# Optimization experiments

Hardware: AMD Instinct MI355X
Metric: run time of the kernel (lower is better)

## Reference

```python
import jax, jax.numpy as jnp
import numpy as np

D_MODEL = 1024
NUM_HEADS = 16
D_K = D_MODEL // NUM_HEADS


def setup_inputs() -> dict:
    key = jax.random.key(0)
    ks = jax.random.split(key, 9)
    B, S = 2, 2048
    s_in = 1.0 / np.sqrt(D_MODEL)
    x = jax.random.normal(ks[0], (B, S, D_MODEL), dtype=jnp.float32)
    # Linear weights stored as (in_features, out_features): y = x @ W + b
    Wq = jax.random.uniform(ks[1], (D_MODEL, D_MODEL), jnp.float32, -s_in, s_in)
    bq = jax.random.uniform(ks[2], (D_MODEL,), jnp.float32, -s_in, s_in)
    Wk = jax.random.uniform(ks[3], (D_MODEL, D_K), jnp.float32, -s_in, s_in)
    bk = jax.random.uniform(ks[4], (D_K,), jnp.float32, -s_in, s_in)
    Wv = jax.random.uniform(ks[5], (D_MODEL, D_K), jnp.float32, -s_in, s_in)
    bv = jax.random.uniform(ks[6], (D_K,), jnp.float32, -s_in, s_in)
    Wo = jax.random.uniform(ks[7], (D_MODEL, D_MODEL), jnp.float32, -s_in, s_in)
    bo = jax.random.uniform(ks[8], (D_MODEL,), jnp.float32, -s_in, s_in)
    return {"x": x, "Wq": Wq, "bq": bq, "Wk": Wk, "bk": bk,
            "Wv": Wv, "bv": bv, "Wo": Wo, "bo": bo}


def reference(x, Wq, bq, Wk, bk, Wv, bv, Wo, bo):
    B, S, _ = x.shape
    H, Dk = NUM_HEADS, D_K
    # Projections
    Q = (x @ Wq + bq).reshape(B, S, H, Dk).transpose(0, 2, 1, 3)  # [B,H,S,Dk]
    K = x @ Wk + bk                                               # [B,S,Dk] single KV head
    V = x @ Wv + bv                                               # [B,S,Dk]
    # Scores: query heads broadcast against the single shared KV head
    scores = jnp.einsum('bhqd,bkd->bhqk', Q, K) / jnp.sqrt(jnp.float32(Dk))
    attn = jax.nn.softmax(scores, axis=-1)                        # [B,H,S,S]
    out = jnp.einsum('bhqk,bkd->bhqd', attn, V)                   # [B,H,S,Dk]
    out = out.transpose(0, 2, 1, 3).reshape(B, S, H * Dk)         # [B,S,d_model]
    return out @ Wo + bo
```

## Files before the change

kernel.cpp:

```cpp
#include <hip/hip_runtime.h>

typedef __attribute__((ext_vector_type(8))) short bf16x8;
typedef __attribute__((ext_vector_type(4))) float f32x4;
typedef __attribute__((ext_vector_type(16))) float f32x16;
typedef __attribute__((ext_vector_type(4))) unsigned short ushort4v;

#define QSCALE 0.1803368801111204f

__device__ __forceinline__ unsigned short f2bf(float f) {
  union { float f; unsigned int u; } x; x.f = f;
  unsigned int u = x.u;
  unsigned int r = (u + 0x7fffu + ((u >> 16) & 1u)) >> 16;
  return (unsigned short)r;
}

__global__ __launch_bounds__(256) void cvt_bf16_kernel(
    const float* __restrict__ in, unsigned short* __restrict__ out, int n) {
  int i = (blockIdx.x * 256 + threadIdx.x) * 4;
  if (i + 3 < n) {
    float4 v = *(const float4*)(in + i);
    ushort4v o = { f2bf(v.x), f2bf(v.y), f2bf(v.z), f2bf(v.w) };
    *(ushort4v*)(out + i) = o;
  }
}

__global__ __launch_bounds__(256) void transpose_cvt_fused(
    const float* __restrict__ Wq, const float* __restrict__ Wk,
    const float* __restrict__ Wv, const float* __restrict__ Wo,
    unsigned short* __restrict__ QKVt, unsigned short* __restrict__ Wot) {
  __shared__ float t[32][33];
  int z = blockIdx.z;
  const float* src;
  unsigned short* dst;
  int C, rowoff;
  if (z == 0)      { src = Wq; dst = QKVt; C = 1024; rowoff = 0; }
  else if (z == 1) { src = Wk; dst = QKVt; C = 64;   rowoff = 1024; }
  else if (z == 2) { src = Wv; dst = QKVt; C = 64;   rowoff = 1088; }
  else             { src = Wo; dst = Wot;  C = 1024; rowoff = 0; }
  int c0 = blockIdx.x * 32, r0 = blockIdx.y * 32;
  if (c0 >= C) return;
  int tx = threadIdx.x & 31, ty = threadIdx.x >> 5;
#pragma unroll
  for (int i = 0; i < 32; i += 8)
    t[ty + i][tx] = src[(size_t)(r0 + ty + i) * C + c0 + tx];
  __syncthreads();
#pragma unroll
  for (int i = 0; i < 32; i += 8)
    dst[(size_t)(rowoff + c0 + ty + i) * 1024 + r0 + tx] = f2bf(t[tx][ty + i]);
}

__global__ __launch_bounds__(256) void make_vt_kernel(
    const unsigned short* __restrict__ QKV, unsigned short* __restrict__ Vt) {
  __shared__ unsigned short t[32][33];
  int b = blockIdx.z;
  int s0 = blockIdx.x * 32, d0 = blockIdx.y * 32;
  int tx = threadIdx.x & 31, ty = threadIdx.x >> 5;
#pragma unroll
  for (int i = 0; i < 32; i += 8)
    t[ty + i][tx] = QKV[(size_t)(b * 2048 + s0 + ty + i) * 1152 + 1088 + d0 + tx];
  __syncthreads();
#pragma unroll
  for (int i = 0; i < 32; i += 8)
    Vt[((size_t)b * 64 + d0 + ty + i) * 2048 + s0 + tx] = t[tx][ty + i];
}

template <typename OutT, bool QKVMODE>
__global__ __launch_bounds__(256) void gemm_bf16_kernel(
    const unsigned short* __restrict__ A, const unsigned short* __restrict__ Bt,
    const float* __restrict__ b0, const float* __restrict__ b1,
    const float* __restrict__ b2, OutT* __restrict__ C, int M, int N, int K) {
  constexpr int LS = 40;
  __shared__ unsigned short As[2][128 * LS];
  __shared__ unsigned short Bs[2][128 * LS];
  int tid = threadIdx.x;
  int wid = tid >> 6, lane = tid & 63;
  int l15 = lane & 15, quad = lane >> 4;
  int m0 = blockIdx.x * 128, n0 = blockIdx.y * 128;
  int mw = (wid >> 1) * 64, nw = (wid & 1) * 64;
  f32x4 acc[4][4];
#pragma unroll
  for (int i = 0; i < 4; i++)
#pragma unroll
    for (int j = 0; j < 4; j++)
#pragma unroll
      for (int e = 0; e < 4; ++e) acc[i][j][e] = 0.f;

  int arow = tid >> 2, akc = (tid & 3) * 8;
  const unsigned short* Ag = A + (size_t)(m0 + arow) * K + akc;
  const unsigned short* Bg = Bt + (size_t)(n0 + arow) * K + akc;
  bf16x8 ar0 = *(const bf16x8*)(Ag);
  bf16x8 ar1 = *(const bf16x8*)(Ag + (size_t)64 * K);
  bf16x8 br0 = *(const bf16x8*)(Bg);
  bf16x8 br1 = *(const bf16x8*)(Bg + (size_t)64 * K);

  for (int k0 = 0; k0 < K; k0 += 32) {
    unsigned short* Asb = As[(k0 >> 5) & 1];
    unsigned short* Bsb = Bs[(k0 >> 5) & 1];
    *(bf16x8*)(Asb + arow * LS + akc) = ar0;
    *(bf16x8*)(Asb + (arow + 64) * LS + akc) = ar1;
    *(bf16x8*)(Bsb + arow * LS + akc) = br0;
    *(bf16x8*)(Bsb + (arow + 64) * LS + akc) = br1;
    __syncthreads();
    if (k0 + 32 < K) {
      ar0 = *(const bf16x8*)(Ag + k0 + 32);
      ar1 = *(const bf16x8*)(Ag + (size_t)64 * K + k0 + 32);
      br0 = *(const bf16x8*)(Bg + k0 + 32);
      br1 = *(const bf16x8*)(Bg + (size_t)64 * K + k0 + 32);
    }
    bf16x8 af[4], bfr[4];
#pragma unroll
    for (int t = 0; t < 4; ++t)
      af[t] = *(const bf16x8*)(Asb + (mw + t * 16 + l15) * LS + quad * 8);
#pragma unroll
    for (int t = 0; t < 4; ++t)
      bfr[t] = *(const bf16x8*)(Bsb + (nw + t * 16 + l15) * LS + quad * 8);
#pragma unroll
    for (int mt = 0; mt < 4; ++mt)
#pragma unroll
      for (int nt = 0; nt < 4; ++nt)
        acc[mt][nt] = __builtin_amdgcn_mfma_f32_16x16x32_bf16(
            af[mt], bfr[nt], acc[mt][nt], 0, 0, 0);
  }
#pragma unroll
  for (int mt = 0; mt < 4; ++mt)
#pragma unroll
    for (int nt = 0; nt < 4; ++nt) {
      int col = n0 + nw + nt * 16 + l15;
      float bias, cs;
      if constexpr (QKVMODE) {
        bias = (col < 1024) ? b0[col] : ((col < 1088) ? b1[col - 1024] : b2[col - 1088]);
        cs = (col < 1024) ? QSCALE : 1.0f;
      } else {
        bias = b0[col];
        cs = 1.0f;
      }
#pragma unroll
      for (int r = 0; r < 4; ++r) {
        int row = m0 + mw + mt * 16 + quad * 4 + r;
        float v = (acc[mt][nt][r] + bias) * cs;
        if constexpr (sizeof(OutT) == 2)
          C[(size_t)row * N + col] = f2bf(v);
        else
          C[(size_t)row * N + col] = v;
      }
    }
}

__global__ __launch_bounds__(256) void flash_attn_kernel(
    const unsigned short* __restrict__ QKV,
    const unsigned short* __restrict__ Vt,
    unsigned short* __restrict__ AO) {
  constexpr int S = 2048, LDQ = 1152;
  constexpr int PK = 72;
  constexpr int PP = 72;
  __shared__ unsigned short Ks[2][64 * PK];
  __shared__ unsigned short Vs[2][64 * PK];
  __shared__ unsigned short Ps[4][32 * PP];
  int tid = threadIdx.x;
  int wid = tid >> 6, lane = tid & 63;
  int l31 = lane & 31, half = lane >> 5;
  int q0 = blockIdx.x * 128, h = blockIdx.y, b = blockIdx.z;

  const unsigned short* Qb =
      QKV + (size_t)(b * S + q0 + wid * 32 + l31) * LDQ + h * 64 + half * 8;
  bf16x8 qf[4];
#pragma unroll
  for (int f = 0; f < 4; ++f) qf[f] = *(const bf16x8*)(Qb + f * 16);

  int srow = tid >> 3, skc = (tid & 7) * 8;
  const unsigned short* Kg = QKV + ((size_t)(b * S + srow) * LDQ + 1024 + skc);
  const unsigned short* Vg = Vt + ((size_t)(b * 64 + srow) * 2048 + skc);
  unsigned short* Pw = Ps[wid];

  f32x16 oacc[2];
  float rs[16];
#pragma unroll
  for (int r = 0; r < 16; ++r) {
    rs[r] = 0.f;
    oacc[0][r] = 0.f;
    oacc[1][r] = 0.f;
  }

  bf16x8 kr0 = *(const bf16x8*)(Kg);
  bf16x8 kr1 = *(const bf16x8*)(Kg + (size_t)32 * LDQ);
  bf16x8 vr0 = *(const bf16x8*)(Vg);
  bf16x8 vr1 = *(const bf16x8*)(Vg + (size_t)32 * 2048);

  for (int kb = 0; kb < S; kb += 64) {
    unsigned short* Ksb = Ks[(kb >> 6) & 1];
    unsigned short* Vsb = Vs[(kb >> 6) & 1];
    *(bf16x8*)(Ksb + srow * PK + skc) = kr0;
    *(bf16x8*)(Ksb + (srow + 32) * PK + skc) = kr1;
    *(bf16x8*)(Vsb + srow * PK + skc) = vr0;
    *(bf16x8*)(Vsb + (srow + 32) * PK + skc) = vr1;
    __syncthreads();
    if (kb + 64 < S) {
      kr0 = *(const bf16x8*)(Kg + (size_t)(kb + 64) * LDQ);
      kr1 = *(const bf16x8*)(Kg + (size_t)(kb + 96) * LDQ);
      vr0 = *(const bf16x8*)(Vg + kb + 64);
      vr1 = *(const bf16x8*)(Vg + (size_t)32 * 2048 + kb + 64);
    }

#pragma unroll
    for (int n2 = 0; n2 < 2; ++n2) {
      f32x16 sacc;
#pragma unroll
      for (int i = 0; i < 16; ++i) sacc[i] = 0.f;
#pragma unroll
      for (int s = 0; s < 4; ++s) {
        bf16x8 kf = *(const bf16x8*)(Ksb + (n2 * 32 + l31) * PK + s * 16 + half * 8);
        sacc = __builtin_amdgcn_mfma_f32_32x32x16_bf16(qf[s], kf, sacc, 0, 0, 0);
      }
#pragma unroll
      for (int r = 0; r < 16; ++r) {
        float p = __builtin_amdgcn_exp2f(sacc[r]);
        rs[r] += p;
        int row = (r & 3) + 8 * (r >> 2) + 4 * half;
        Pw[row * PP + n2 * 32 + l31] = f2bf(p);
      }
    }

    bf16x8 pf[4];
#pragma unroll
    for (int s = 0; s < 4; ++s)
      pf[s] = *(const bf16x8*)(Pw + l31 * PP + s * 16 + half * 8);
#pragma unroll
    for (int d2 = 0; d2 < 2; ++d2)
#pragma unroll
      for (int s = 0; s < 4; ++s) {
        bf16x8 vf = *(const bf16x8*)(Vsb + (d2 * 32 + l31) * PK + s * 16 + half * 8);
        oacc[d2] = __builtin_amdgcn_mfma_f32_32x32x16_bf16(pf[s], vf, oacc[d2], 0, 0, 0);
      }
  }

  float inv[16];
#pragma unroll
  for (int r = 0; r < 16; ++r) {
    float s = rs[r];
    s += __shfl_xor(s, 1, 32);
    s += __shfl_xor(s, 2, 32);
    s += __shfl_xor(s, 4, 32);
    s += __shfl_xor(s, 8, 32);
    s += __shfl_xor(s, 16, 32);
    inv[r] = 1.0f / s;
  }

  unsigned short* Ob = AO + (size_t)(b * S + q0 + wid * 32) * 1024 + h * 64;
#pragma unroll
  for (int d2 = 0; d2 < 2; ++d2)
#pragma unroll
    for (int r = 0; r < 16; ++r) {
      int row = (r & 3) + 8 * (r >> 2) + 4 * half;
      Ob[(size_t)row * 1024 + d2 * 32 + l31] = f2bf(oacc[d2][r] * inv[r]);
    }
}

extern "C" void kernel_launch(void* const* d_in, const int* in_sizes, int n_in,
                              void* d_out, int out_size, void* d_ws, size_t ws_size,
                              hipStream_t stream) {
  const float* x  = (const float*)d_in[0];
  const float* Wq = (const float*)d_in[1];
  const float* bq = (const float*)d_in[2];
  const float* Wk = (const float*)d_in[3];
  const float* bk = (const float*)d_in[4];
  const float* Wv = (const float*)d_in[5];
  const float* bv = (const float*)d_in[6];
  const float* Wo = (const float*)d_in[7];
  const float* bo = (const float*)d_in[8];
  float* out = (float*)d_out;

  constexpr int B = 2, S = 2048, D = 1024, Dk = 64, H = 16;
  constexpr int M = B * S;
  constexpr int NQKV = D + 2 * Dk;

  char* ws = (char*)d_ws;
  unsigned short* xb   = (unsigned short*)ws; ws += (size_t)M * D * 2;
  unsigned short* QKVt = (unsigned short*)ws; ws += (size_t)NQKV * D * 2;
  unsigned short* Wot  = (unsigned short*)ws; ws += (size_t)D * D * 2;
  unsigned short* QKV  = (unsigned short*)ws; ws += (size_t)M * NQKV * 2;
  unsigned short* Vtb  = (unsigned short*)ws; ws += (size_t)B * Dk * S * 2;
  unsigned short* AO   = (unsigned short*)ws; ws += (size_t)M * D * 2;

  cvt_bf16_kernel<<<M * D / 1024, 256, 0, stream>>>(x, xb, M * D);
  transpose_cvt_fused<<<dim3(32, 32, 4), 256, 0, stream>>>(Wq, Wk, Wv, Wo, QKVt, Wot);

  gemm_bf16_kernel<unsigned short, true><<<dim3(M / 128, NQKV / 128), 256, 0, stream>>>(
      xb, QKVt, bq, bk, bv, QKV, M, NQKV, D);
  make_vt_kernel<<<dim3(S / 32, Dk / 32, B), 256, 0, stream>>>(QKV, Vtb);

  flash_attn_kernel<<<dim3(S / 128, H, B), 256, 0, stream>>>(QKV, Vtb, AO);

  gemm_bf16_kernel<float, false><<<dim3(M / 128, D / 128), 256, 0, stream>>>(
      AO, Wot, bo, nullptr, nullptr, out, M, D, D);
}
```

Baseline: 195.4 us.

## Keep P in registers via transposed MFMA, fuse V-transpose and x conversion

The attention kernel swaps MFMA operand order so S^T lands with keys spread across lanes. The P fragments for the PV MFMA are then built from registers with one cross-half shuffle, which removes the shared-memory P staging and the per-row shuffle reductions for the row sums. The V transpose is folded into the QKV GEMM epilogue as extra scattered stores, and the x-to-bf16 conversion is merged into the weight transpose kernel. This cuts two launches and LDS traffic, at the cost of uncoalesced Vt stores and more register pressure.

```diff
diff --git a/kernel.cpp b/kernel.cpp
--- a/kernel.cpp
+++ b/kernel.cpp
@@ -1,4 +1,5 @@
 #include <hip/hip_runtime.h>
+#include <hip/hip_bf16.h>
 
 typedef __attribute__((ext_vector_type(8))) short bf16x8;
 typedef __attribute__((ext_vector_type(4))) float f32x4;
@@ -14,22 +15,30 @@
   return (unsigned short)r;
 }
 
-__global__ __launch_bounds__(256) void cvt_bf16_kernel(
-    const float* __restrict__ in, unsigned short* __restrict__ out, int n) {
-  int i = (blockIdx.x * 256 + threadIdx.x) * 4;
-  if (i + 3 < n) {
-    float4 v = *(const float4*)(in + i);
-    ushort4v o = { f2bf(v.x), f2bf(v.y), f2bf(v.z), f2bf(v.w) };
-    *(ushort4v*)(out + i) = o;
-  }
-}
-
-__global__ __launch_bounds__(256) void transpose_cvt_fused(
+__device__ __forceinline__ unsigned int bfpack2(float a, float b) {
+  union { __hip_bfloat162 h; unsigned int u; } c;
+  c.h = __float22bfloat162_rn(make_float2(a, b));
+  return c.u;
+}
+
+__global__ __launch_bounds__(256) void prep_kernel(
+    const float* __restrict__ x,
     const float* __restrict__ Wq, const float* __restrict__ Wk,
     const float* __restrict__ Wv, const float* __restrict__ Wo,
+    unsigned short* __restrict__ xb,
     unsigned short* __restrict__ QKVt, unsigned short* __restrict__ Wot) {
+  int z = blockIdx.z;
+  if (z == 4) {
+    size_t base = ((size_t)(blockIdx.y * 32 + blockIdx.x)) * 4096 + threadIdx.x * 16;
+#pragma unroll
+    for (int c = 0; c < 4; ++c) {
+      float4 v = *(const float4*)(x + base + c * 4);
+      ushort4v o = { f2bf(v.x), f2bf(v.y), f2bf(v.z), f2bf(v.w) };
+      *(ushort4v*)(xb + base + c * 4) = o;
+    }
+    return;
+  }
   __shared__ float t[32][33];
-  int z = blockIdx.z;
   const float* src;
   unsigned short* dst;
   int C, rowoff;
@@ -49,26 +58,12 @@
     dst[(size_t)(rowoff + c0 + ty + i) * 1024 + r0 + tx] = f2bf(t[tx][ty + i]);
 }
 
-__global__ __launch_bounds__(256) void make_vt_kernel(
-    const unsigned short* __restrict__ QKV, unsigned short* __restrict__ Vt) {
-  __shared__ unsigned short t[32][33];
-  int b = blockIdx.z;
-  int s0 = blockIdx.x * 32, d0 = blockIdx.y * 32;
-  int tx = threadIdx.x & 31, ty = threadIdx.x >> 5;
-#pragma unroll
-  for (int i = 0; i < 32; i += 8)
-    t[ty + i][tx] = QKV[(size_t)(b * 2048 + s0 + ty + i) * 1152 + 1088 + d0 + tx];
-  __syncthreads();
-#pragma unroll
-  for (int i = 0; i < 32; i += 8)
-    Vt[((size_t)b * 64 + d0 + ty + i) * 2048 + s0 + tx] = t[tx][ty + i];
-}
-
 template <typename OutT, bool QKVMODE>
 __global__ __launch_bounds__(256) void gemm_bf16_kernel(
     const unsigned short* __restrict__ A, const unsigned short* __restrict__ Bt,
     const float* __restrict__ b0, const float* __restrict__ b1,
-    const float* __restrict__ b2, OutT* __restrict__ C, int M, int N, int K) {
+    const float* __restrict__ b2, OutT* __restrict__ C,
+    unsigned short* __restrict__ Vt, int M, int N, int K) {
   constexpr int LS = 40;
   __shared__ unsigned short As[2][128 * LS];
   __shared__ unsigned short Bs[2][128 * LS];
@@ -142,6 +137,11 @@
           C[(size_t)row * N + col] = f2bf(v);
         else
           C[(size_t)row * N + col] = v;
+        if constexpr (QKVMODE) {
+          if (col >= 1088)
+            Vt[((size_t)(row >> 11) * 64 + (col - 1088)) * 2048 + (row & 2047)] =
+                f2bf(v);
+        }
       }
     }
 }
@@ -152,10 +152,8 @@
     unsigned short* __restrict__ AO) {
   constexpr int S = 2048, LDQ = 1152;
   constexpr int PK = 72;
-  constexpr int PP = 72;
   __shared__ unsigned short Ks[2][64 * PK];
   __shared__ unsigned short Vs[2][64 * PK];
-  __shared__ unsigned short Ps[4][32 * PP];
   int tid = threadIdx.x;
   int wid = tid >> 6, lane = tid & 63;
   int l31 = lane & 31, half = lane >> 5;
@@ -170,16 +168,11 @@
   int srow = tid >> 3, skc = (tid & 7) * 8;
   const unsigned short* Kg = QKV + ((size_t)(b * S + srow) * LDQ + 1024 + skc);
   const unsigned short* Vg = Vt + ((size_t)(b * 64 + srow) * 2048 + skc);
-  unsigned short* Pw = Ps[wid];
 
   f32x16 oacc[2];
-  float rs[16];
-#pragma unroll
-  for (int r = 0; r < 16; ++r) {
-    rs[r] = 0.f;
-    oacc[0][r] = 0.f;
-    oacc[1][r] = 0.f;
-  }
+#pragma unroll
+  for (int r = 0; r < 16; ++r) { oacc[0][r] = 0.f; oacc[1][r] = 0.f; }
+  float rsacc = 0.f;
 
   bf16x8 kr0 = *(const bf16x8*)(Kg);
   bf16x8 kr1 = *(const bf16x8*)(Kg + (size_t)32 * LDQ);
@@ -201,57 +194,63 @@
       vr1 = *(const bf16x8*)(Vg + (size_t)32 * 2048 + kb + 64);
     }
 
+    unsigned int pk[2][8];
 #pragma unroll
     for (int n2 = 0; n2 < 2; ++n2) {
       f32x16 sacc;
 #pragma unroll
       for (int i = 0; i < 16; ++i) sacc[i] = 0.f;
 #pragma unroll
-      for (int s = 0; s < 4; ++s) {
-        bf16x8 kf = *(const bf16x8*)(Ksb + (n2 * 32 + l31) * PK + s * 16 + half * 8);
-        sacc = __builtin_amdgcn_mfma_f32_32x32x16_bf16(qf[s], kf, sacc, 0, 0, 0);
-      }
-#pragma unroll
-      for (int r = 0; r < 16; ++r) {
-        float p = __builtin_amdgcn_exp2f(sacc[r]);
-        rs[r] += p;
-        int row = (r & 3) + 8 * (r >> 2) + 4 * half;
-        Pw[row * PP + n2 * 32 + l31] = f2bf(p);
-      }
-    }
-
-    bf16x8 pf[4];
-#pragma unroll
-    for (int s = 0; s < 4; ++s)
-      pf[s] = *(const bf16x8*)(Pw + l31 * PP + s * 16 + half * 8);
+      for (int s4 = 0; s4 < 4; ++s4) {
+        bf16x8 kf = *(const bf16x8*)(Ksb + (n2 * 32 + l31) * PK + s4 * 16 + half * 8);
+        sacc = __builtin_amdgcn_mfma_f32_32x32x16_bf16(kf, qf[s4], sacc, 0, 0, 0);
+      }
+#pragma unroll
+      for (int v = 0; v < 8; ++v) {
+        float p0 = __builtin_amdgcn_exp2f(sacc[2 * v]);
+        float p1 = __builtin_amdgcn_exp2f(sacc[2 * v + 1]);
+        rsacc += p0 + p1;
+        pk[n2][v] = bfpack2(p0, p1);
+      }
+    }
+    unsigned int other[2][8];
+#pragma unroll
+    for (int n2 = 0; n2 < 2; ++n2)
+#pragma unroll
+      for (int v = 0; v < 8; ++v) other[n2][v] = __shfl_xor(pk[n2][v], 32);
+
+    bf16x8 pfr[4];
+#pragma unroll
+    for (int s = 0; s < 4; ++s) {
+      int n2 = s >> 1, vb = 4 * (s & 1);
+      union { bf16x8 v; unsigned int u[4]; } fr;
+      fr.u[0] = half ? other[n2][vb + 2] : pk[n2][vb + 0];
+      fr.u[1] = half ? other[n2][vb + 3] : pk[n2][vb + 1];
+      fr.u[2] = half ? pk[n2][vb + 2]    : other[n2][vb + 0];
+      fr.u[3] = half ? pk[n2][vb + 3]    : other[n2][vb + 1];
+      pfr[s] = fr.v;
+    }
+
 #pragma unroll
     for (int d2 = 0; d2 < 2; ++d2)
 #pragma unroll
       for (int s = 0; s < 4; ++s) {
         bf16x8 vf = *(const bf16x8*)(Vsb + (d2 * 32 + l31) * PK + s * 16 + half * 8);
-        oacc[d2] = __builtin_amdgcn_mfma_f32_32x32x16_bf16(pf[s], vf, oacc[d2], 0, 0, 0);
+        oacc[d2] = __builtin_amdgcn_mfma_f32_32x32x16_bf16(vf, pfr[s], oacc[d2], 0, 0, 0);
       }
   }
 
-  float inv[16];
-#pragma unroll
-  for (int r = 0; r < 16; ++r) {
-    float s = rs[r];
-    s += __shfl_xor(s, 1, 32);
-    s += __shfl_xor(s, 2, 32);
-    s += __shfl_xor(s, 4, 32);
-    s += __shfl_xor(s, 8, 32);
-    s += __shfl_xor(s, 16, 32);
-    inv[r] = 1.0f / s;
-  }
-
-  unsigned short* Ob = AO + (size_t)(b * S + q0 + wid * 32) * 1024 + h * 64;
+  float inv = 1.0f / (rsacc + __shfl_xor(rsacc, 32));
+
+  unsigned short* Ob = AO + (size_t)(b * S + q0 + wid * 32 + l31) * 1024 + h * 64;
 #pragma unroll
   for (int d2 = 0; d2 < 2; ++d2)
 #pragma unroll
-    for (int r = 0; r < 16; ++r) {
-      int row = (r & 3) + 8 * (r >> 2) + 4 * half;
-      Ob[(size_t)row * 1024 + d2 * 32 + l31] = f2bf(oacc[d2][r] * inv[r]);
+    for (int g = 0; g < 4; ++g) {
+      union { ushort4v s4; unsigned int u[2]; } w;
+      w.u[0] = bfpack2(oacc[d2][4 * g + 0] * inv, oacc[d2][4 * g + 1] * inv);
+      w.u[1] = bfpack2(oacc[d2][4 * g + 2] * inv, oacc[d2][4 * g + 3] * inv);
+      *(ushort4v*)(Ob + d2 * 32 + 8 * g + 4 * half) = w.s4;
     }
 }
 
@@ -281,15 +280,13 @@
   unsigned short* Vtb  = (unsigned short*)ws; ws += (size_t)B * Dk * S * 2;
   unsigned short* AO   = (unsigned short*)ws; ws += (size_t)M * D * 2;
 
-  cvt_bf16_kernel<<<M * D / 1024, 256, 0, stream>>>(x, xb, M * D);
-  transpose_cvt_fused<<<dim3(32, 32, 4), 256, 0, stream>>>(Wq, Wk, Wv, Wo, QKVt, Wot);
+  prep_kernel<<<dim3(32, 32, 5), 256, 0, stream>>>(x, Wq, Wk, Wv, Wo, xb, QKVt, Wot);
 
   gemm_bf16_kernel<unsigned short, true><<<dim3(M / 128, NQKV / 128), 256, 0, stream>>>(
-      xb, QKVt, bq, bk, bv, QKV, M, NQKV, D);
-  make_vt_kernel<<<dim3(S / 32, Dk / 32, B), 256, 0, stream>>>(QKV, Vtb);
+      xb, QKVt, bq, bk, bv, QKV, Vtb, M, NQKV, D);
 
   flash_attn_kernel<<<dim3(S / 128, H, B), 256, 0, stream>>>(QKV, Vtb, AO);
 
   gemm_bf16_kernel<float, false><<<dim3(M / 128, D / 128), 256, 0, stream>>>(
-      AO, Wot, bo, nullptr, nullptr, out, M, D, D);
-}
+      AO, Wot, bo, nullptr, nullptr, out, nullptr, M, D, D);
+}
```

Result: no change. 194.3 us (-0.6%).
